# Kernel optimization log

Measured on AMD Instinct MI355X. Metric: run time of the kernel, lower is better.

The kernel has to match this reference:

```python
import jax, jax.numpy as jnp
import numpy as np

N, D = 16384, 32            # nodes, max neighbors (0-padded)
INP, U = 256, 128           # input_units, units
R, ENT = 8, 8               # relations, entity types (relation/entity id 0 = padding for relations)


def setup_inputs() -> dict:
    key = jax.random.key(0)
    ks = jax.random.split(key, 12)
    s = 0.05  # scale learned params for numerical sanity (torch init is raw randn)
    return {
        "node_state": jax.random.normal(ks[0], (N, INP), dtype=jnp.float32),
        "adjacency": jax.random.randint(ks[1], (N, D), 0, N + 1, dtype=jnp.int32),  # 0 = pad row
        "point_enc": jax.random.randint(ks[2], (N,), 0, ENT, dtype=jnp.int32),
        "relation_enc": jax.random.randint(ks[3], (N, D), 0, R, dtype=jnp.int32),   # 0 = pad edge
        "point_enc_w": jax.random.normal(ks[4], (ENT, INP, U), dtype=jnp.float32) * s,
        "relation_enc_w": jax.random.normal(ks[5], (R, U, U), dtype=jnp.float32) * s,
        "q_w": jax.random.normal(ks[6], (U, U), dtype=jnp.float32) * s,
        "k_w": jax.random.normal(ks[7], (U, U), dtype=jnp.float32) * s,
        "v_w": jax.random.normal(ks[8], (U, U), dtype=jnp.float32) * s,
        "fc_w": jax.random.normal(ks[9], (U, U), dtype=jnp.float32) * s,
        "fc_b": jax.random.normal(ks[10], (U,), dtype=jnp.float32) * s,
    }


def reference(node_state, adjacency, point_enc, relation_enc,
              point_enc_w, relation_enc_w, q_w, k_w, v_w, fc_w, fc_b):
    ent, inp, u = point_enc_w.shape
    r_cnt = relation_enc_w.shape[0]
    dt = node_state.dtype

    # center = node_state @ point_enc_w[point_enc]; loop over small fixed entity set
    # to avoid materializing an (N, INP, U) gathered weight tensor.
    center = jnp.zeros((node_state.shape[0], u), dtype=dt)
    for e in range(ent):
        center = center + jnp.where(point_enc[:, None] == e,
                                    node_state @ point_enc_w[e], 0.0)

    # prepend zero row: adjacency index 0 == padding neighbor
    padded = jnp.concatenate([jnp.zeros((1, u), dtype=dt), center], axis=0)  # (N+1, U)
    x = padded[adjacency]  # (N, D, U) gathered neighbor embeddings

    # neighbors = x @ relation_enc_w[relation_enc]; per-relation GEMM + mask
    # (same math as the per-edge gathered matmul, without the E*U*U blowup)
    neighbors = jnp.zeros_like(x)
    for r in range(r_cnt):
        neighbors = neighbors + jnp.where(relation_enc[..., None] == r,
                                          jnp.einsum('ndu,uv->ndv', x, relation_enc_w[r]), 0.0)

    scale = u ** 0.5
    q = (center @ q_w) / scale                               # (N, U)
    k = jnp.einsum('ndu,uv->ndv', neighbors, k_w) / scale    # (N, D, U)
    v = jnp.einsum('ndu,uv->ndv', neighbors, v_w)            # (N, D, U)

    scores = jnp.einsum('nu,ndu->nd', q, k)                  # (N, D)
    scores = jnp.where(relation_enc == 0, jnp.asarray(-1e9, dt), scores)
    attn = jax.nn.softmax(scores, axis=-1)                   # over neighbors
    agg = jnp.einsum('nd,ndu->nu', attn, v)                  # (N, U)

    return center + jax.nn.relu(agg @ fc_w + fc_b)           # (N, U)
```

## Files before the change

### kernel.cpp

```cpp
#include <hip/hip_runtime.h>

#define NNODE 16384
#define DD 32
#define INPC 256
#define UC 128
#define RC 8
#define EC 8

typedef __attribute__((ext_vector_type(8))) short short8;
typedef __attribute__((ext_vector_type(4))) float float4v;
typedef __attribute__((ext_vector_type(4))) unsigned uint4v;

__device__ __forceinline__ unsigned short f2bf(float f) {
    unsigned u = __builtin_bit_cast(unsigned, f);
    unsigned r = (u + 0x7FFFu + ((u >> 16) & 1u)) >> 16;
    return (unsigned short)r;
}
__device__ __forceinline__ float bf2f(unsigned short s) { return __builtin_bit_cast(float, (unsigned)s << 16); }

template <int CTRL>
__device__ __forceinline__ float dppq(float x) {
    return __builtin_bit_cast(float,
        __builtin_amdgcn_mov_dpp(__builtin_bit_cast(int, x), CTRL, 0xF, 0xF, true));
}
#define DPP_XOR1 0xB1
#define DPP_XOR2 0x4E

__device__ __forceinline__ short8 ld8bf(const float* p) {
    float4 v0 = *(const float4*)p;
    float4 v1 = *(const float4*)(p + 4);
    short8 a;
    a[0] = (short)f2bf(v0.x); a[1] = (short)f2bf(v0.y);
    a[2] = (short)f2bf(v0.z); a[3] = (short)f2bf(v0.w);
    a[4] = (short)f2bf(v1.x); a[5] = (short)f2bf(v1.y);
    a[6] = (short)f2bf(v1.z); a[7] = (short)f2bf(v1.w);
    return a;
}

__device__ __forceinline__ int bfrag_idx(int k, int col, int nct) {
    int ks = k >> 5, ct = col >> 4;
    int l = (((k >> 3) & 3) << 4) | (col & 15);
    return (((ks * nct + ct) << 6) + l) * 8 + (k & 7);
}

__global__ void k_setup(const float* __restrict__ pew, const float* __restrict__ qw,
                        const float* __restrict__ kw, const float* __restrict__ relw,
                        const float* __restrict__ vw, const float* __restrict__ fcw,
                        const int* __restrict__ pe,
                        unsigned short* __restrict__ pewfrag,
                        unsigned short* __restrict__ BallQfrag, unsigned short* __restrict__ RVFfrag,
                        int* __restrict__ blockhist) {
    __shared__ unsigned short stage_s[128 * 132];
    __shared__ unsigned short mat_s[16 * 136];
    __shared__ int hh[8];
    int b = blockIdx.x;
    if (b < 1024) {
        int id = b * 256 + threadIdx.x;
        int e = id >> 15, k = (id >> 7) & 255, col = id & 127;
        pewfrag[(e << 15) + bfrag_idx(k, col, 8)] = f2bf(pew[id]);
        return;
    }
    if (b < 1088) {
        int pb = b - 1024;
        int r = pb & 7, i0 = (pb >> 3) * 16;
        int w = threadIdx.x >> 6, l = threadIdx.x & 63;
        int mrow = l & 15, kgrp = (l >> 4) << 3;
        const float* R = relw + r * (UC * UC);

        float4v accP[2] = {};
        #pragma unroll
        for (int ks = 0; ks < 4; ++ks) {
            short8 a = ld8bf(&qw[(i0 + mrow) * UC + ks * 32 + kgrp]);
            #pragma unroll
            for (int ci = 0; ci < 2; ++ci) {
                int ct = w * 2 + ci;
                short8 bf = ld8bf(&kw[(ct * 16 + mrow) * UC + ks * 32 + kgrp]);
                accP[ci] = __builtin_amdgcn_mfma_f32_16x16x32_bf16(a, bf, accP[ci], 0, 0, 0);
            }
        }
        #pragma unroll
        for (int ci = 0; ci < 2; ++ci)
            #pragma unroll
            for (int reg = 0; reg < 4; ++reg) {
                int row = ((l >> 4) << 2) + reg;
                int col = (w * 2 + ci) * 16 + mrow;
                mat_s[row * 136 + col] = f2bf(accP[ci][reg] * (1.0f / 128.0f));
            }
        for (int it = 0; it < 16; ++it) {
            int idx = it * 256 + threadIdx.x;
            int row = idx >> 5, col = (idx & 31) * 4;
            float4 v = *(const float4*)&vw[row * UC + col];
            uint2 o;
            o.x = (unsigned)f2bf(v.x) | ((unsigned)f2bf(v.y) << 16);
            o.y = (unsigned)f2bf(v.z) | ((unsigned)f2bf(v.w) << 16);
            *(uint2*)&stage_s[row * 132 + col] = o;
        }
        __syncthreads();

        float4v accM[2] = {}, accV[2] = {};
        #pragma unroll
        for (int ks = 0; ks < 4; ++ks) {
            short8 aM = *(const short8*)&mat_s[mrow * 136 + ks * 32 + kgrp];
            short8 aV = ld8bf(&R[(i0 + mrow) * UC + ks * 32 + kgrp]);
            #pragma unroll
            for (int ci = 0; ci < 2; ++ci) {
                int ct = w * 2 + ci;
                short8 bM = ld8bf(&R[(ct * 16 + mrow) * UC + ks * 32 + kgrp]);
                accM[ci] = __builtin_amdgcn_mfma_f32_16x16x32_bf16(aM, bM, accM[ci], 0, 0, 0);
                uint4v pv;
                #pragma unroll
                for (int jp = 0; jp < 4; ++jp) {
                    unsigned e0 = stage_s[(ks * 32 + kgrp + jp * 2) * 132 + ct * 16 + mrow];
                    unsigned e1 = stage_s[(ks * 32 + kgrp + jp * 2 + 1) * 132 + ct * 16 + mrow];
                    pv[jp] = e0 | (e1 << 16);
                }
                accV[ci] = __builtin_amdgcn_mfma_f32_16x16x32_bf16(
                    aV, __builtin_bit_cast(short8, pv), accV[ci], 0, 0, 0);
            }
        }
        #pragma unroll
        for (int ci = 0; ci < 2; ++ci)
            #pragma unroll
            for (int reg = 0; reg < 4; ++reg) {
                int i = i0 + ((l >> 4) << 2) + reg;
                int col = r * 128 + (w * 2 + ci) * 16 + mrow;
                BallQfrag[bfrag_idx(i, col, 64)] = f2bf(accM[ci][reg]);
            }
        __syncthreads();
        #pragma unroll
        for (int ci = 0; ci < 2; ++ci)
            #pragma unroll
            for (int reg = 0; reg < 4; ++reg)
                mat_s[(((l >> 4) << 2) + reg) * 136 + (w * 2 + ci) * 16 + mrow] = f2bf(accV[ci][reg]);
        for (int it = 0; it < 16; ++it) {
            int idx = it * 256 + threadIdx.x;
            int row = idx >> 5, col = (idx & 31) * 4;
            float4 v = *(const float4*)&fcw[row * UC + col];
            uint2 o;
            o.x = (unsigned)f2bf(v.x) | ((unsigned)f2bf(v.y) << 16);
            o.y = (unsigned)f2bf(v.z) | ((unsigned)f2bf(v.w) << 16);
            *(uint2*)&stage_s[row * 132 + col] = o;
        }
        __syncthreads();

        float4v accF[2] = {};
        #pragma unroll
        for (int ks = 0; ks < 4; ++ks) {
            short8 aF = *(const short8*)&mat_s[mrow * 136 + ks * 32 + kgrp];
            #pragma unroll
            for (int ci = 0; ci < 2; ++ci) {
                int ct = w * 2 + ci;
                uint4v pv;
                #pragma unroll
                for (int jp = 0; jp < 4; ++jp) {
                    unsigned e0 = stage_s[(ks * 32 + kgrp + jp * 2) * 132 + ct * 16 + mrow];
                    unsigned e1 = stage_s[(ks * 32 + kgrp + jp * 2 + 1) * 132 + ct * 16 + mrow];
                    pv[jp] = e0 | (e1 << 16);
                }
                accF[ci] = __builtin_amdgcn_mfma_f32_16x16x32_bf16(
                    aF, __builtin_bit_cast(short8, pv), accF[ci], 0, 0, 0);
            }
        }
        #pragma unroll
        for (int ci = 0; ci < 2; ++ci)
            #pragma unroll
            for (int reg = 0; reg < 4; ++reg) {
                int i = i0 + ((l >> 4) << 2) + reg;
                int col = (w * 2 + ci) * 16 + mrow;
                RVFfrag[bfrag_idx(r * 128 + i, col, 8)] = f2bf(accF[ci][reg]);
            }
        return;
    }
    {
        int hb = b - 1088;
        if (threadIdx.x < 8) hh[threadIdx.x] = 0;
        __syncthreads();
        atomicAdd(&hh[pe[hb * 256 + threadIdx.x]], 1);
        __syncthreads();
        if (threadIdx.x < 8) blockhist[hb * 8 + threadIdx.x] = hh[threadIdx.x];
    }
}

__global__ void k_scatter(const int* __restrict__ pe, const int* __restrict__ blockhist,
                          int* __restrict__ list, int* __restrict__ cnt, int* __restrict__ basep) {
    __shared__ int boff[8];
    __shared__ int totS[8], exS[8];
    __shared__ int wavecnt[4 * 8];
    int t = threadIdx.x, w = t >> 6, l = t & 63;
    if (w == 0) {
        #pragma unroll
        for (int e = 0; e < 8; ++e) {
            int h = blockhist[l * 8 + e];
            int pref = h;
            #pragma unroll
            for (int off = 1; off < 64; off <<= 1) {
                int v = __shfl_up(pref, off, 64);
                pref += (l >= off) ? v : 0;
            }
            if (l == (int)blockIdx.x) exS[e] = pref - h;
            if (l == 63) totS[e] = pref;
        }
    }
    __syncthreads();
    if (t == 0) {
        int run = 0;
        #pragma unroll
        for (int e = 0; e < 8; ++e) {
            boff[e] = run + exS[e];
            if (blockIdx.x == 0) { basep[e] = run; cnt[e] = totS[e]; }
            run += totS[e];
        }
    }
    __syncthreads();
    int n = blockIdx.x * 256 + t;
    int e = pe[n];
    unsigned long long mymask = 0;
    #pragma unroll
    for (int r = 0; r < 8; ++r) {
        unsigned long long m = __ballot(e == r);
        if (e == r) mymask = m;
        if (l == r) wavecnt[w * 8 + r] = (int)__popcll(m);
    }
    __syncthreads();
    int off = 0;
    for (int w2 = 0; w2 < w; ++w2) off += wavecnt[w2 * 8 + e];
    unsigned long long ltmask = (1ull << l) - 1ull;
    int rank = (int)__popcll(mymask & ltmask);
    list[boff[e] + off + rank] = n;
}

__global__ __launch_bounds__(256, 4)
void k_center(const float* __restrict__ ns, const unsigned short* __restrict__ pewfrag,
              const int* __restrict__ list, const int* __restrict__ cnt,
              const int* __restrict__ base, unsigned short* __restrict__ center_bf) {
    int e = blockIdx.y;
    int c = cnt[e];
    int start = blockIdx.x * 16;
    if (start >= c) return;
    int w = threadIdx.x >> 6, l = threadIdx.x & 63;

    int rid = list[base[e] + min(start + (l & 15), c - 1)];

    float4v acc[2] = {};
    const unsigned short* pf = pewfrag + ((size_t)e << 15);
    #pragma unroll
    for (int ks = 0; ks < 8; ++ks) {
        short8 a = ld8bf(&ns[(size_t)rid * 256 + ks * 32 + ((l >> 4) << 3)]);
        #pragma unroll
        for (int ci = 0; ci < 2; ++ci) {
            int ct = w * 2 + ci;
            short8 b = *(const short8*)&pf[(((ks * 8 + ct) << 6) + l) * 8];
            acc[ci] = __builtin_amdgcn_mfma_f32_16x16x32_bf16(a, b, acc[ci], 0, 0, 0);
        }
    }
    #pragma unroll
    for (int reg = 0; reg < 4; ++reg) {
        int row16 = start + ((l >> 4) << 2) + reg;
        if (row16 < c) {
            int gid = list[base[e] + row16];
            #pragma unroll
            for (int ci = 0; ci < 2; ++ci)
                center_bf[(size_t)gid * 128 + (w * 2 + ci) * 16 + (l & 15)] = f2bf(acc[ci][reg]);
        }
    }
}

#define QSTRIDE 1096
__global__ __launch_bounds__(256, 4)
void k_final(const unsigned short* __restrict__ center_bf,
             const unsigned short* __restrict__ BallQfrag,
             const unsigned short* __restrict__ RVFfrag,
             const int* __restrict__ adj, const int* __restrict__ rel,
             const float* __restrict__ fcb, float* __restrict__ out) {
    __shared__ unsigned short qlds[16 * QSTRIDE];
    int w = threadIdx.x >> 6, l = threadIdx.x & 63;
    int n0 = blockIdx.x * 16;

    int pk[4][2];
    #pragma unroll
    for (int q = 0; q < 4; ++q) {
        int n = n0 + w * 4 + q;
        #pragma unroll
        for (int t = 0; t < 2; ++t) {
            int ai = adj[n * DD + t * 16 + (l & 15)];
            int rv = rel[n * DD + t * 16 + (l & 15)];
            int rr = ai > 0 ? ai - 1 : 0;
            pk[q][t] = (rr << 5) | (rv << 1) | (ai != 0 ? 1 : 0);
        }
    }

    short8 xp[2][4];
    #pragma unroll
    for (int t = 0; t < 2; ++t)
        #pragma unroll
        for (int ks = 0; ks < 4; ++ks)
            xp[t][ks] = *(const short8*)&center_bf[(size_t)(pk[0][t] >> 5) * 128
                                                   + ks * 32 + ((l >> 4) << 3)];

    {
        short8 a[4];
        #pragma unroll
        for (int ks = 0; ks < 4; ++ks)
            a[ks] = *(const short8*)&center_bf[(size_t)(n0 + (l & 15)) * 128 + ks * 32 + ((l >> 4) << 3)];
        for (int ci = 0; ci < 16; ++ci) {
            int ct = w * 16 + ci;
            float4v acc = {};
            #pragma unroll
            for (int ks = 0; ks < 4; ++ks) {
                short8 b = *(const short8*)&BallQfrag[(((ks * 64 + ct) << 6) + l) * 8];
                acc = __builtin_amdgcn_mfma_f32_16x16x32_bf16(a[ks], b, acc, 0, 0, 0);
            }
            int r = ct >> 3;
            int ch = (ct & 7) * 16 + (l & 15);
            #pragma unroll
            for (int reg = 0; reg < 4; ++reg) {
                int rn = ((l >> 4) << 2) + reg;
                qlds[rn * QSTRIDE + r * 136 + ch] = f2bf(acc[reg]);
            }
        }
    }
    __syncthreads();

    #pragma unroll
    for (int q = 0; q < 4; ++q) {
        int tn = w * 4 + q;
        int p0 = pk[q][0], p1 = pk[q][1];
        int rv0 = (p0 >> 1) & 7, rv1 = (p1 >> 1) & 7;
        int va0 = p0 & 1, va1 = p1 & 1;

        float4v sc[2] = {};
        #pragma unroll
        for (int ks = 0; ks < 4; ++ks) {
            short8 qb = *(const short8*)&qlds[tn * QSTRIDE + (l & 7) * 136 + ks * 32 + ((l >> 4) << 3)];
            sc[0] = __builtin_amdgcn_mfma_f32_16x16x32_bf16(qb, xp[0][ks], sc[0], 0, 0, 0);
            sc[1] = __builtin_amdgcn_mfma_f32_16x16x32_bf16(qb, xp[1][ks], sc[1], 0, 0, 0);
        }

        int rsel = (l & 32) ? (p1 >> 5) : (p0 >> 5);
        int rows[8];
        #pragma unroll
        for (int jj = 0; jj < 8; ++jj)
            rows[jj] = __shfl(rsel, (l & 48) | (((l >> 4) & 1) * 8 + jj), 64);
        unsigned short g0[4][8];
        #pragma unroll
        for (int ct = 0; ct < 4; ++ct)
            #pragma unroll
            for (int jj = 0; jj < 8; ++jj)
                g0[ct][jj] = center_bf[(size_t)rows[jj] * 128 + ct * 16 + (l & 15)];

        if (q < 3) {
            #pragma unroll
            for (int t = 0; t < 2; ++t)
                #pragma unroll
                for (int ks = 0; ks < 4; ++ks)
                    xp[t][ks] = *(const short8*)&center_bf[(size_t)(pk[q + 1][t] >> 5) * 128
                                                           + ks * 32 + ((l >> 4) << 3)];
        }

        float sel0, sel1;
        {
            int r = rv0;
            float v01 = (r & 1) ? sc[0][1] : sc[0][0];
            float v23 = (r & 1) ? sc[0][3] : sc[0][2];
            float regv = (r & 2) ? v23 : v01;
            float s = __shfl(regv, ((r >> 2) << 4) | (l & 15), 64);
            if (!va0) s = 0.f;
            if (r == 0) s = -1e9f;
            sel0 = fminf(s, 60.f);
        }
        {
            int r = rv1;
            float v01 = (r & 1) ? sc[1][1] : sc[1][0];
            float v23 = (r & 1) ? sc[1][3] : sc[1][2];
            float regv = (r & 2) ? v23 : v01;
            float s = __shfl(regv, ((r >> 2) << 4) | (l & 15), 64);
            if (!va1) s = 0.f;
            if (r == 0) s = -1e9f;
            sel1 = fminf(s, 60.f);
        }

        float at0 = __expf(sel0);
        float at1 = __expf(sel1);
        float sm = at0 + at1;
        sm += dppq<DPP_XOR1>(sm);
        sm += dppq<DPP_XOR2>(sm);
        sm += __shfl_xor(sm, 4, 64);
        sm += __shfl_xor(sm, 8, 64);
        float inv = 1.0f / fmaxf(sm, 1e-30f);
        at0 *= inv; at1 *= inv;
        if (!va0) at0 = 0.f;
        if (!va1) at1 = 0.f;

        unsigned md0 = (unsigned)f2bf(at0) | ((unsigned)rv0 << 16);
        unsigned md1 = (unsigned)f2bf(at1) | ((unsigned)rv1 << 16);
        unsigned mdsel = (l >= 32) ? md1 : md0;
        unsigned aw[4];
        #pragma unroll
        for (int jp = 0; jp < 4; ++jp) {
            unsigned m0 = __shfl(mdsel, (l & 48) | (((l >> 4) & 1) * 8 + jp * 2), 64);
            unsigned m1 = __shfl(mdsel, (l & 48) | (((l >> 4) & 1) * 8 + jp * 2 + 1), 64);
            unsigned s0 = ((m0 >> 16) == (unsigned)(l & 15)) ? (m0 & 0xFFFFu) : 0u;
            unsigned s1 = ((m1 >> 16) == (unsigned)(l & 15)) ? (m1 & 0xFFFFu) : 0u;
            aw[jp] = s0 | (s1 << 16);
        }
        uint4v av = {aw[0], aw[1], aw[2], aw[3]};
        short8 afrag = __builtin_bit_cast(short8, av);

        #pragma unroll
        for (int ct = 0; ct < 4; ++ct) {
            uint4v bv = {(unsigned)g0[ct][0] | ((unsigned)g0[ct][1] << 16),
                         (unsigned)g0[ct][2] | ((unsigned)g0[ct][3] << 16),
                         (unsigned)g0[ct][4] | ((unsigned)g0[ct][5] << 16),
                         (unsigned)g0[ct][6] | ((unsigned)g0[ct][7] << 16)};
            float4v zc = {};
            float4v acc = __builtin_amdgcn_mfma_f32_16x16x32_bf16(
                afrag, __builtin_bit_cast(short8, bv), zc, 0, 0, 0);
            if (l < 32) {
                int rbase = (l >> 4) << 2;
                #pragma unroll
                for (int reg = 0; reg < 4; ++reg)
                    qlds[tn * QSTRIDE + (rbase + reg) * 136 + ct * 16 + (l & 15)] = f2bf(acc[reg]);
            }
        }

        unsigned short g1[4][8];
        #pragma unroll
        for (int c2 = 0; c2 < 4; ++c2)
            #pragma unroll
            for (int jj = 0; jj < 8; ++jj)
                g1[c2][jj] = center_bf[(size_t)rows[jj] * 128 + (c2 + 4) * 16 + (l & 15)];
        #pragma unroll
        for (int c2 = 0; c2 < 4; ++c2) {
            int ct = c2 + 4;
            uint4v bv = {(unsigned)g1[c2][0] | ((unsigned)g1[c2][1] << 16),
                         (unsigned)g1[c2][2] | ((unsigned)g1[c2][3] << 16),
                         (unsigned)g1[c2][4] | ((unsigned)g1[c2][5] << 16),
                         (unsigned)g1[c2][6] | ((unsigned)g1[c2][7] << 16)};
            float4v zc = {};
            float4v acc = __builtin_amdgcn_mfma_f32_16x16x32_bf16(
                afrag, __builtin_bit_cast(short8, bv), zc, 0, 0, 0);
            if (l < 32) {
                int rbase = (l >> 4) << 2;
                #pragma unroll
                for (int reg = 0; reg < 4; ++reg)
                    qlds[tn * QSTRIDE + (rbase + reg) * 136 + ct * 16 + (l & 15)] = f2bf(acc[reg]);
            }
        }
    }
    __syncthreads();

    {
        float4v acc[2] = {};
        #pragma unroll 4
        for (int ks = 0; ks < 32; ++ks) {
            short8 a = *(const short8*)&qlds[(l & 15) * QSTRIDE + (ks >> 2) * 136
                                             + (ks & 3) * 32 + ((l >> 4) << 3)];
            #pragma unroll
            for (int ci = 0; ci < 2; ++ci) {
                int ct = w * 2 + ci;
                short8 b = *(const short8*)&RVFfrag[(((ks * 8 + ct) << 6) + l) * 8];
                acc[ci] = __builtin_amdgcn_mfma_f32_16x16x32_bf16(a, b, acc[ci], 0, 0, 0);
            }
        }
        #pragma unroll
        for (int ci = 0; ci < 2; ++ci) {
            int ct = w * 2 + ci;
            int col = ct * 16 + (l & 15);
            float bb = fcb[col];
            #pragma unroll
            for (int reg = 0; reg < 4; ++reg) {
                int n = n0 + ((l >> 4) << 2) + reg;
                float v = acc[ci][reg] + bb;
                v = v > 0.f ? v : 0.f;
                out[(size_t)n * 128 + col] = bf2f(center_bf[(size_t)n * 128 + col]) + v;
            }
        }
    }
}

extern "C" void kernel_launch(void* const* d_in, const int* in_sizes, int n_in,
                              void* d_out, int out_size, void* d_ws, size_t ws_size,
                              hipStream_t stream) {
    const float* node_state = (const float*)d_in[0];
    const int*   adjacency  = (const int*)d_in[1];
    const int*   point_enc  = (const int*)d_in[2];
    const int*   relation   = (const int*)d_in[3];
    const float* pew        = (const float*)d_in[4];
    const float* relw       = (const float*)d_in[5];
    const float* qw         = (const float*)d_in[6];
    const float* kw         = (const float*)d_in[7];
    const float* vw         = (const float*)d_in[8];
    const float* fcw        = (const float*)d_in[9];
    const float* fcb        = (const float*)d_in[10];
    float* out = (float*)d_out;

    char* ws = (char*)d_ws;
    unsigned short* BallQfrag = (unsigned short*)ws;  ws += 128 * 1024 * 2;
    unsigned short* RVFfrag   = (unsigned short*)ws;  ws += 1024 * 128 * 2;
    unsigned short* center_bf = (unsigned short*)ws;  ws += (size_t)NNODE * 128 * 2;
    unsigned short* pewfrag   = (unsigned short*)ws;  ws += 8 * 32768 * 2;
    int* blockhist            = (int*)ws;             ws += 64 * 8 * 4;
    int* cnt                  = (int*)ws;             ws += 32;
    int* basep                = (int*)ws;             ws += 32;
    int* list                 = (int*)ws;             ws += NNODE * 4;

    k_setup<<<1152, 256, 0, stream>>>(pew, qw, kw, relw, vw, fcw, point_enc,
                                      pewfrag, BallQfrag, RVFfrag, blockhist);
    k_scatter<<<64, 256, 0, stream>>>(point_enc, blockhist, list, cnt, basep);
    k_center<<<dim3(192, 8), 256, 0, stream>>>(node_state, pewfrag, list, cnt, basep, center_bf);
    k_final<<<NNODE / 16, 256, 0, stream>>>(center_bf, BallQfrag, RVFfrag,
                                            adjacency, relation, fcb, out);
}
```

Baseline: 160.2 us.

## Replace entity sort/scatter with masked per-entity MFMA loop in center kernel

```diff
diff --git a/kernel.cpp b/kernel.cpp
--- a/kernel.cpp
+++ b/kernel.cpp
@@ -46,22 +46,22 @@
 __global__ void k_setup(const float* __restrict__ pew, const float* __restrict__ qw,
                         const float* __restrict__ kw, const float* __restrict__ relw,
                         const float* __restrict__ vw, const float* __restrict__ fcw,
-                        const int* __restrict__ pe,
                         unsigned short* __restrict__ pewfrag,
-                        unsigned short* __restrict__ BallQfrag, unsigned short* __restrict__ RVFfrag,
-                        int* __restrict__ blockhist) {
+                        unsigned short* __restrict__ BallQfrag, unsigned short* __restrict__ RVFfrag) {
     __shared__ unsigned short stage_s[128 * 132];
     __shared__ unsigned short mat_s[16 * 136];
-    __shared__ int hh[8];
     int b = blockIdx.x;
-    if (b < 1024) {
-        int id = b * 256 + threadIdx.x;
-        int e = id >> 15, k = (id >> 7) & 255, col = id & 127;
-        pewfrag[(e << 15) + bfrag_idx(k, col, 8)] = f2bf(pew[id]);
+    if (b < 256) {
+        #pragma unroll
+        for (int it = 0; it < 4; ++it) {
+            int id = it * 65536 + b * 256 + threadIdx.x;
+            int e = id >> 15, k = (id >> 7) & 255, col = id & 127;
+            pewfrag[(e << 15) + bfrag_idx(k, col, 8)] = f2bf(pew[id]);
+        }
         return;
     }
-    if (b < 1088) {
-        int pb = b - 1024;
+    {
+        int pb = b - 256;
         int r = pb & 7, i0 = (pb >> 3) * 16;
         int w = threadIdx.x >> 6, l = threadIdx.x & 63;
         int mrow = l & 15, kgrp = (l >> 4) << 3;
@@ -169,99 +169,44 @@
                 int col = (w * 2 + ci) * 16 + mrow;
                 RVFfrag[bfrag_idx(r * 128 + i, col, 8)] = f2bf(accF[ci][reg]);
             }
-        return;
-    }
-    {
-        int hb = b - 1088;
-        if (threadIdx.x < 8) hh[threadIdx.x] = 0;
-        __syncthreads();
-        atomicAdd(&hh[pe[hb * 256 + threadIdx.x]], 1);
-        __syncthreads();
-        if (threadIdx.x < 8) blockhist[hb * 8 + threadIdx.x] = hh[threadIdx.x];
-    }
-}
-
-__global__ void k_scatter(const int* __restrict__ pe, const int* __restrict__ blockhist,
-                          int* __restrict__ list, int* __restrict__ cnt, int* __restrict__ basep) {
-    __shared__ int boff[8];
-    __shared__ int totS[8], exS[8];
-    __shared__ int wavecnt[4 * 8];
-    int t = threadIdx.x, w = t >> 6, l = t & 63;
-    if (w == 0) {
-        #pragma unroll
-        for (int e = 0; e < 8; ++e) {
-            int h = blockhist[l * 8 + e];
-            int pref = h;
-            #pragma unroll
-            for (int off = 1; off < 64; off <<= 1) {
-                int v = __shfl_up(pref, off, 64);
-                pref += (l >= off) ? v : 0;
-            }
-            if (l == (int)blockIdx.x) exS[e] = pref - h;
-            if (l == 63) totS[e] = pref;
-        }
-    }
-    __syncthreads();
-    if (t == 0) {
-        int run = 0;
-        #pragma unroll
-        for (int e = 0; e < 8; ++e) {
-            boff[e] = run + exS[e];
-            if (blockIdx.x == 0) { basep[e] = run; cnt[e] = totS[e]; }
-            run += totS[e];
-        }
-    }
-    __syncthreads();
-    int n = blockIdx.x * 256 + t;
-    int e = pe[n];
-    unsigned long long mymask = 0;
-    #pragma unroll
-    for (int r = 0; r < 8; ++r) {
-        unsigned long long m = __ballot(e == r);
-        if (e == r) mymask = m;
-        if (l == r) wavecnt[w * 8 + r] = (int)__popcll(m);
-    }
-    __syncthreads();
-    int off = 0;
-    for (int w2 = 0; w2 < w; ++w2) off += wavecnt[w2 * 8 + e];
-    unsigned long long ltmask = (1ull << l) - 1ull;
-    int rank = (int)__popcll(mymask & ltmask);
-    list[boff[e] + off + rank] = n;
+    }
 }
 
 __global__ __launch_bounds__(256, 4)
 void k_center(const float* __restrict__ ns, const unsigned short* __restrict__ pewfrag,
-              const int* __restrict__ list, const int* __restrict__ cnt,
-              const int* __restrict__ base, unsigned short* __restrict__ center_bf) {
-    int e = blockIdx.y;
-    int c = cnt[e];
-    int start = blockIdx.x * 16;
-    if (start >= c) return;
+              const int* __restrict__ pe, unsigned short* __restrict__ center_bf) {
     int w = threadIdx.x >> 6, l = threadIdx.x & 63;
-
-    int rid = list[base[e] + min(start + (l & 15), c - 1)];
+    int n0 = blockIdx.x * 16;
+    int row = n0 + (l & 15);
+    int ent = pe[row];
+
+    short8 a[8];
+    #pragma unroll
+    for (int ks = 0; ks < 8; ++ks)
+        a[ks] = ld8bf(&ns[(size_t)row * 256 + ks * 32 + ((l >> 4) << 3)]);
 
     float4v acc[2] = {};
-    const unsigned short* pf = pewfrag + ((size_t)e << 15);
-    #pragma unroll
-    for (int ks = 0; ks < 8; ++ks) {
-        short8 a = ld8bf(&ns[(size_t)rid * 256 + ks * 32 + ((l >> 4) << 3)]);
-        #pragma unroll
-        for (int ci = 0; ci < 2; ++ci) {
-            int ct = w * 2 + ci;
-            short8 b = *(const short8*)&pf[(((ks * 8 + ct) << 6) + l) * 8];
-            acc[ci] = __builtin_amdgcn_mfma_f32_16x16x32_bf16(a, b, acc[ci], 0, 0, 0);
+    short8 z = {};
+    for (int e = 0; e < 8; ++e) {
+        if (!__any(ent == e)) continue;
+        const unsigned short* pf = pewfrag + ((size_t)e << 15);
+        #pragma unroll
+        for (int ks = 0; ks < 8; ++ks) {
+            short8 am = (ent == e) ? a[ks] : z;
+            #pragma unroll
+            for (int ci = 0; ci < 2; ++ci) {
+                int ct = w * 2 + ci;
+                short8 b = *(const short8*)&pf[(((ks * 8 + ct) << 6) + l) * 8];
+                acc[ci] = __builtin_amdgcn_mfma_f32_16x16x32_bf16(am, b, acc[ci], 0, 0, 0);
+            }
         }
     }
     #pragma unroll
     for (int reg = 0; reg < 4; ++reg) {
-        int row16 = start + ((l >> 4) << 2) + reg;
-        if (row16 < c) {
-            int gid = list[base[e] + row16];
-            #pragma unroll
-            for (int ci = 0; ci < 2; ++ci)
-                center_bf[(size_t)gid * 128 + (w * 2 + ci) * 16 + (l & 15)] = f2bf(acc[ci][reg]);
-        }
+        int orow = n0 + ((l >> 4) << 2) + reg;
+        #pragma unroll
+        for (int ci = 0; ci < 2; ++ci)
+            center_bf[(size_t)orow * 128 + (w * 2 + ci) * 16 + (l & 15)] = f2bf(acc[ci][reg]);
     }
 }
 
@@ -499,15 +444,10 @@
     unsigned short* RVFfrag   = (unsigned short*)ws;  ws += 1024 * 128 * 2;
     unsigned short* center_bf = (unsigned short*)ws;  ws += (size_t)NNODE * 128 * 2;
     unsigned short* pewfrag   = (unsigned short*)ws;  ws += 8 * 32768 * 2;
-    int* blockhist            = (int*)ws;             ws += 64 * 8 * 4;
-    int* cnt                  = (int*)ws;             ws += 32;
-    int* basep                = (int*)ws;             ws += 32;
-    int* list                 = (int*)ws;             ws += NNODE * 4;
-
-    k_setup<<<1152, 256, 0, stream>>>(pew, qw, kw, relw, vw, fcw, point_enc,
-                                      pewfrag, BallQfrag, RVFfrag, blockhist);
-    k_scatter<<<64, 256, 0, stream>>>(point_enc, blockhist, list, cnt, basep);
-    k_center<<<dim3(192, 8), 256, 0, stream>>>(node_state, pewfrag, list, cnt, basep, center_bf);
+
+    k_setup<<<320, 256, 0, stream>>>(pew, qw, kw, relw, vw, fcw,
+                                     pewfrag, BallQfrag, RVFfrag);
+    k_center<<<NNODE / 16, 256, 0, stream>>>(node_state, pewfrag, point_enc, center_bf);
     k_final<<<NNODE / 16, 256, 0, stream>>>(center_bf, BallQfrag, RVFfrag,
                                             adjacency, relation, fcb, out);
 }
```

Result: slower. 163.7 us (+2.2%).
